# Optimization experiments

Measured on AMD Instinct MI355X. Metric: run time of the kernel, lower is better.

## Reference

```python
import jax, jax.numpy as jnp
import numpy as np

NUM_PTS = 4
N_OFF = 4


def inverse_sigmoid(x, eps=1e-5):
    x = jnp.clip(x, 0.0, 1.0)
    return jnp.log(jnp.clip(x, eps, None) / jnp.clip(1.0 - x, eps, None))


def uniform_flat_indices(T, H, W, n):
    # torch: linspace(hop/2, D-1-hop/2, n).round().long(), meshed over (t,h,w)
    def ax(D):
        hop = D / n
        return jnp.round(jnp.linspace(hop / 2.0, D - 1.0 - hop / 2.0, n)).astype(jnp.int32)
    ti, hi, wi = ax(T), ax(H), ax(W)
    return ((ti[:, None, None] * H + hi[None, :, None]) * W + wi[None, None, :]).reshape(-1)


def _normalized_thw(idx, T, H, W):
    wn = (idx % W).astype(jnp.float32) / (W - 1)
    hn = ((idx // W) % H).astype(jnp.float32) / (H - 1)
    tn = (idx // (W * H)).astype(jnp.float32) / (T - 1)
    return jnp.stack([tn, hn, wn], axis=-1)


def grid_sample_3d(inp, grid):
    # Matches torch F.grid_sample 5D, bilinear, padding zeros, align_corners=False.
    # inp: (N,C,D,H,W); grid: (N,Do,Ho,Wo,3) with grid[...,0]=x->W, 1=y->H, 2=z->D
    N, C, D, H, W = inp.shape
    Do, Ho, Wo = grid.shape[1:4]
    P = Do * Ho * Wo
    g = grid.reshape(N, P, 3)
    ix = ((g[..., 0] + 1.0) * W - 1.0) * 0.5
    iy = ((g[..., 1] + 1.0) * H - 1.0) * 0.5
    iz = ((g[..., 2] + 1.0) * D - 1.0) * 0.5
    x0 = jnp.floor(ix); y0 = jnp.floor(iy); z0 = jnp.floor(iz)
    fx = ix - x0; fy = iy - y0; fz = iz - z0
    x0i = x0.astype(jnp.int32); y0i = y0.astype(jnp.int32); z0i = z0.astype(jnp.int32)
    inp_flat = inp.reshape(N, C, D * H * W)
    out = jnp.zeros((N, C, P), inp.dtype)
    for dz in (0, 1):
        for dy in (0, 1):
            for dx in (0, 1):
                xi = x0i + dx; yi = y0i + dy; zi = z0i + dz
                w = (fx if dx else 1.0 - fx) * (fy if dy else 1.0 - fy) * (fz if dz else 1.0 - fz)
                valid = (xi >= 0) & (xi < W) & (yi >= 0) & (yi < H) & (zi >= 0) & (zi < D)
                flat = (jnp.clip(zi, 0, D - 1) * H + jnp.clip(yi, 0, H - 1)) * W + jnp.clip(xi, 0, W - 1)
                vals = jnp.take_along_axis(inp_flat, jnp.broadcast_to(flat[:, None, :], (N, C, P)), axis=2)
                out = out + vals * (w * valid.astype(inp.dtype))[:, None, :]
    return out.reshape(N, C, Do, Ho, Wo)


def forward(features, pos, W1, b1, W2, b2, Wn, bn, Wl, bl, Woff, boff, Ww, bw, gamma, beta):
    B, C, T, H, Wd, L = features.shape
    THW = T * H * Wd
    No = N_OFF
    N = NUM_PTS ** 3
    d = C // No
    BLNo = B * L * No

    flat = uniform_flat_indices(T, H, Wd, NUM_PTS)                    # (N,)
    ind_pts = jnp.broadcast_to(flat[None, None, :], (B, L, N))

    feats_l = jnp.transpose(features, (0, 5, 2, 3, 4, 1)).reshape(B, L, THW, C)
    pos_l = jnp.transpose(pos, (0, 5, 2, 3, 4, 1)).reshape(B, L, THW, C)
    sampled_pts = feats_l[:, :, flat, :]                              # (B,L,N,C)
    sampled_pos = pos_l[:, :, flat, :]
    glob = jnp.transpose(jnp.mean(features, axis=(2, 3, 4)), (0, 2, 1))  # (B,L,C)
    glob = jnp.broadcast_to(glob[:, :, None, :], (B, L, N, C))

    off_src = jnp.concatenate([sampled_pts, sampled_pos, glob], axis=-1)
    off_src = jax.nn.relu(off_src @ W1 + b1)
    off_src = jax.nn.relu(off_src @ W2 + b2)                          # (B,L,N,C)

    nxt = off_src @ Wn + bn                                           # (B,L,N,3)
    w_l = jax.nn.softmax(off_src @ Wl + bl, axis=-1)                  # (B,L,N,L)

    osr = off_src.reshape(B, L, N, No, d).transpose(0, 1, 3, 2, 4).reshape(BLNo, N, d)
    offset = osr @ Woff + boff                                        # (BLNo,N,3)
    w_o = jax.nn.softmax(osr @ Ww + bw, axis=-1)[..., 1:]             # (BLNo,N,1)

    # --- build flow field: identity grid with sampled coords scattered in ---
    idx = jnp.broadcast_to(ind_pts[:, :, None, :], (B, L, No, N)).reshape(BLNo, N)
    thw = _normalized_thw(idx, T, H, Wd)
    samp = jax.nn.sigmoid(inverse_sigmoid(thw) + offset) * 2.0 - 1.0  # (BLNo,N,3)
    mesh = jnp.stack(jnp.meshgrid(jnp.linspace(-1.0, 1.0, T), jnp.linspace(-1.0, 1.0, H), jnp.linspace(-1.0, 1.0, Wd), indexing='ij'), axis=-1).reshape(THW, 3)
    base = jnp.broadcast_to(mesh[None], (BLNo, THW, 3))
    bI = jnp.arange(BLNo)[:, None]
    flow = base.at[bI, idx].set(samp).reshape(BLNo, T, H, Wd, 3)

    feats_rep = jnp.transpose(features, (0, 5, 1, 2, 3, 4))           # (B,L,C,T,H,W)
    feats_rep = jnp.broadcast_to(feats_rep[:, :, None], (B, L, No, C, T, H, Wd)).reshape(BLNo, C, T, H, Wd)
    sf = grid_sample_3d(feats_rep, flow)                              # (BLNo,C,T,H,W)
    sf = jnp.transpose(sf, (0, 2, 3, 4, 1))                           # (BLNo,T,H,W,C)

    wo_full = jnp.zeros((BLNo, THW, 1), features.dtype).at[bI, idx].set(w_o).reshape(BLNo, T, H, Wd, 1)
    wsf = (sf * wo_full).reshape(B, L, No, T, H, Wd, C).sum(axis=2)   # (B,L,T,H,W,C)
    feats2 = features + jnp.transpose(wsf, (0, 5, 2, 3, 4, 1))        # (B,C,T,H,W,L)

    # level weights scattered then summed over target-level axis l
    bI2 = jnp.arange(B)[:, None, None]
    lI2 = jnp.arange(L)[None, :, None]
    wl_full = jnp.zeros((B, L, THW, L), features.dtype).at[bI2, lI2, ind_pts].set(w_l)
    wl_sum = wl_full.sum(axis=-1).reshape(B, L, T, H, Wd)             # (B,L,T,H,W)
    feats3 = feats2 * jnp.transpose(wl_sum, (0, 2, 3, 4, 1))[:, None] # broadcast over C

    # LayerNorm over channel dim (transpose(1,-1) in torch)
    x = jnp.transpose(feats3, (0, 5, 2, 3, 4, 1))                     # (B,L,T,H,W,C)
    mu = jnp.mean(x, axis=-1, keepdims=True)
    var = jnp.var(x, axis=-1, keepdims=True)
    xn = (x - mu) * jax.lax.rsqrt(var + 1e-5) * gamma + beta
    feats_out = jnp.transpose(xn, (0, 5, 2, 3, 4, 1))

    # offset_adder -> next flattened indices
    thw2 = _normalized_thw(ind_pts, T, H, Wd)
    disp = jax.nn.sigmoid(inverse_sigmoid(thw2) + nxt)
    scale = jnp.array([T - 1, H - 1, Wd - 1], jnp.float32)
    di = jnp.round(disp * scale).astype(jnp.int32)
    next_ind = H * Wd * di[..., 0] + Wd * di[..., 1] + di[..., 2]
    return feats_out, next_ind


def setup_inputs():
    key = jax.random.key(0)
    ks = jax.random.split(key, 10)
    B, C, T, H, W, L = 1, 256, 8, 32, 32, 4
    s = 0.02
    d = C // N_OFF
    return {
        'features': jax.random.normal(ks[0], (B, C, T, H, W, L), jnp.float32),
        'pos': jax.random.normal(ks[1], (B, C, T, H, W, L), jnp.float32),
        'W1': jax.random.normal(ks[2], (3 * C, C), jnp.float32) * s,
        'b1': jnp.zeros((C,), jnp.float32),
        'W2': jax.random.normal(ks[3], (C, C), jnp.float32) * s,
        'b2': jnp.zeros((C,), jnp.float32),
        'Wn': jax.random.normal(ks[4], (C, 3), jnp.float32) * s,
        'bn': jnp.zeros((3,), jnp.float32),
        'Wl': jax.random.normal(ks[5], (C, L), jnp.float32) * s,
        'bl': jnp.zeros((L,), jnp.float32),
        'Woff': jax.random.normal(ks[6], (d, 3), jnp.float32) * s,
        'boff': jnp.zeros((3,), jnp.float32),
        'Ww': jax.random.normal(ks[7], (d, 2), jnp.float32) * s,
        'bw': jnp.zeros((2,), jnp.float32),
        'gamma': jnp.ones((C,), jnp.float32),
        'beta': jnp.zeros((C,), jnp.float32),
    }


def reference(features, pos, W1, b1, W2, b2, Wn, bn, Wl, bl, Woff, boff, Ww, bw, gamma, beta):
    return forward(features, pos, W1, b1, W2, b2, Wn, bn, Wl, bl, Woff, boff, Ww, bw, gamma, beta)
```

## Files before the change

kernel.cpp:

```cpp
#include <hip/hip_runtime.h>
#include <math.h>

#define CDIM 256
#define TDIM 8
#define HDIM 32
#define WDIM 32
#define LDIM 4
#define THW 8192
#define CSTR 32768
#define NS 64
#define OUT0_SIZE 8388608

__device__ __constant__ int c_ti[4] = {1, 3, 4, 6};
__device__ __constant__ int c_hw[4] = {4, 12, 19, 27};

__device__ __forceinline__ float sigm(float x) { return 1.f / (1.f + expf(-x)); }

__device__ __forceinline__ float wave_sum64(float x) {
#pragma unroll
    for (int s = 32; s > 0; s >>= 1) x += __shfl_xor(x, s, 64);
    return x;
}

__global__ void __launch_bounds__(256)
k_fill_part(const float* __restrict__ feat, const float* __restrict__ beta,
            float* __restrict__ out, float4* __restrict__ partF) {
    int c = blockIdx.x >> 3, part = blockIdx.x & 7;
    float bv = beta[c];
    float4 bf = make_float4(bv, bv, bv, bv);
    const float4* f = (const float4*)(feat + (size_t)c * CSTR) + part * 1024;
    float4* o = (float4*)(out + (size_t)c * CSTR) + part * 1024;
    float4 a = make_float4(0.f, 0.f, 0.f, 0.f);
#pragma unroll
    for (int it = 0; it < 4; ++it) {
        int i = it * 256 + threadIdx.x;
        float4 v = f[i];
        o[i] = bf;
        a.x += v.x; a.y += v.y; a.z += v.z; a.w += v.w;
    }
#pragma unroll
    for (int s = 32; s > 0; s >>= 1) {
        a.x += __shfl_xor(a.x, s, 64);
        a.y += __shfl_xor(a.y, s, 64);
        a.z += __shfl_xor(a.z, s, 64);
        a.w += __shfl_xor(a.w, s, 64);
    }
    __shared__ float4 sw[4];
    if ((threadIdx.x & 63) == 0) sw[threadIdx.x >> 6] = a;
    __syncthreads();
    if (threadIdx.x == 0) {
        float4 r;
        r.x = sw[0].x + sw[1].x + sw[2].x + sw[3].x;
        r.y = sw[0].y + sw[1].y + sw[2].y + sw[3].y;
        r.z = sw[0].z + sw[1].z + sw[2].z + sw[3].z;
        r.w = sw[0].w + sw[1].w + sw[2].w + sw[3].w;
        partF[blockIdx.x] = r;
    }
}

__global__ void __launch_bounds__(256)
k_gather(const float* __restrict__ feat, const float* __restrict__ pos,
         const float4* __restrict__ partF, float* __restrict__ in1T) {
    int m = blockIdx.x, l = m >> 6, n = m & 63;
    int sp = (c_ti[n >> 4] * HDIM + c_hw[(n >> 2) & 3]) * WDIM + c_hw[n & 3];
    int t = threadIdx.x;
    in1T[(size_t)t * 256 + m] = feat[(size_t)t * CSTR + sp * LDIM + l];
    in1T[(size_t)(256 + t) * 256 + m] = pos[(size_t)t * CSTR + sp * LDIM + l];
    float s = 0.f;
#pragma unroll
    for (int p = 0; p < 8; ++p) {
        float4 v = partF[t * 8 + p];
        s += (l == 0) ? v.x : (l == 1) ? v.y : (l == 2) ? v.z : v.w;
    }
    in1T[(size_t)(512 + t) * 256 + m] = s * (1.f / 8192.f);
}

template <int KITER, int WRITE_T>
__global__ void __launch_bounds__(256)
k_gemm(const float* __restrict__ AT, const float* __restrict__ Wt,
       const float* __restrict__ bias, float* __restrict__ outp) {
    __shared__ float sAcc[256][33];
    int mt = blockIdx.x >> 4, jt = blockIdx.x & 15;
    int m0 = mt * 16, j0 = jt * 16;
    int t = threadIdx.x;
    int j8 = t & 7, kq = t >> 3;
    int j = j0 + j8 * 2;
    float acc0[16], acc1[16];
#pragma unroll
    for (int i = 0; i < 16; ++i) { acc0[i] = 0.f; acc1[i] = 0.f; }
#pragma unroll 4
    for (int kk = 0; kk < KITER; ++kk) {
        int k = kq + (kk << 5);
        const float4* ap = (const float4*)(AT + (size_t)k * 256 + m0);
        float av[16];
        ((float4*)av)[0] = ap[0];
        ((float4*)av)[1] = ap[1];
        ((float4*)av)[2] = ap[2];
        ((float4*)av)[3] = ap[3];
        float2 w = *(const float2*)(Wt + (size_t)k * 256 + j);
#pragma unroll
        for (int i = 0; i < 16; ++i) {
            acc0[i] = fmaf(av[i], w.x, acc0[i]);
            acc1[i] = fmaf(av[i], w.y, acc1[i]);
        }
    }
#pragma unroll
    for (int i = 0; i < 16; ++i) {
        sAcc[i * 16 + j8 * 2 + 0][kq] = acc0[i];
        sAcc[i * 16 + j8 * 2 + 1][kq] = acc1[i];
    }
    __syncthreads();
    int i = t >> 4, jj = t & 15;
    float v = bias[j0 + jj];
#pragma unroll
    for (int q = 0; q < 32; ++q) v += sAcc[t][q];
    v = fmaxf(v, 0.f);
    if (WRITE_T)
        outp[(size_t)(j0 + jj) * 256 + m0 + i] = v;
    else
        outp[(size_t)(m0 + i) * 256 + j0 + jj] = v;
}

__global__ void __launch_bounds__(256)
k_heads_sample(const float* __restrict__ feat, const float* __restrict__ osrc,
               const float* __restrict__ Wn, const float* __restrict__ bn,
               const float* __restrict__ Woff, const float* __restrict__ boff,
               const float* __restrict__ Ww, const float* __restrict__ bw,
               const float* __restrict__ gamma, const float* __restrict__ beta,
               float* __restrict__ out, float* __restrict__ next_out) {
    __shared__ float s_samp[4][3];
    __shared__ float s_wo[4];
    __shared__ float s_w[32];
    __shared__ int   s_o[32];
    __shared__ float red1[4], red2[4], redn[3][4];

    int m = blockIdx.x, l = m >> 6, n = m & 63;
    int j = threadIdx.x, o = j >> 6, r = j & 63;

    float v = osrc[(size_t)m * 256 + j];

    float pn0 = wave_sum64(v * Wn[j * 3 + 0]);
    float pn1 = wave_sum64(v * Wn[j * 3 + 1]);
    float pn2 = wave_sum64(v * Wn[j * 3 + 2]);
    if (r == 0) { redn[0][o] = pn0; redn[1][o] = pn1; redn[2][o] = pn2; }

    float po0 = wave_sum64(v * Woff[r * 3 + 0]);
    float po1 = wave_sum64(v * Woff[r * 3 + 1]);
    float po2 = wave_sum64(v * Woff[r * 3 + 2]);
    float z0  = wave_sum64(v * Ww[r * 2 + 0]);
    float z1  = wave_sum64(v * Ww[r * 2 + 1]);

    float tn = (float)c_ti[n >> 4] / 7.f;
    float hn = (float)c_hw[(n >> 2) & 3] / 31.f;
    float wn = (float)c_hw[n & 3] / 31.f;
    float lg0 = logf(tn / (1.f - tn));
    float lg1 = logf(hn / (1.f - hn));
    float lg2 = logf(wn / (1.f - wn));

    if (r == 0) {
        s_samp[o][0] = sigm(lg0 + po0 + boff[0]) * 2.f - 1.f;
        s_samp[o][1] = sigm(lg1 + po1 + boff[1]) * 2.f - 1.f;
        s_samp[o][2] = sigm(lg2 + po2 + boff[2]) * 2.f - 1.f;
        s_wo[o] = 1.f / (1.f + expf((z0 + bw[0]) - (z1 + bw[1])));
    }
    __syncthreads();

    if (j == 0) {
        float t0 = redn[0][0] + redn[0][1] + redn[0][2] + redn[0][3];
        float t1 = redn[1][0] + redn[1][1] + redn[1][2] + redn[1][3];
        float t2 = redn[2][0] + redn[2][1] + redn[2][2] + redn[2][3];
        float d0 = rintf(sigm(lg0 + t0 + bn[0]) * 7.f);
        float d1 = rintf(sigm(lg1 + t1 + bn[1]) * 31.f);
        float d2 = rintf(sigm(lg2 + t2 + bn[2]) * 31.f);
        next_out[m] = 1024.f * d0 + 32.f * d1 + d2;
    }

    if (j < 4) {
        int oo = j;
        float wv = s_wo[oo];
        float g0 = s_samp[oo][0], g1 = s_samp[oo][1], g2 = s_samp[oo][2];
        float ix = ((g0 + 1.f) * 32.f - 1.f) * 0.5f;
        float iy = ((g1 + 1.f) * 32.f - 1.f) * 0.5f;
        float iz = ((g2 + 1.f) * 8.f  - 1.f) * 0.5f;
        float x0f = floorf(ix), y0f = floorf(iy), z0f = floorf(iz);
        float fx = ix - x0f, fy = iy - y0f, fz = iz - z0f;
        int x0 = (int)x0f, y0 = (int)y0f, z0 = (int)z0f;
#pragma unroll
        for (int k = 0; k < 8; ++k) {
            int dx = k & 1, dy = (k >> 1) & 1, dz = k >> 2;
            int xi = x0 + dx, yi = y0 + dy, zi = z0 + dz;
            float w = (dx ? fx : 1.f - fx) * (dy ? fy : 1.f - fy) * (dz ? fz : 1.f - fz);
            bool valid = (xi >= 0) && (xi < WDIM) && (yi >= 0) && (yi < HDIM) && (zi >= 0) && (zi < TDIM);
            int xc = min(max(xi, 0), WDIM - 1);
            int yc = min(max(yi, 0), HDIM - 1);
            int zc = min(max(zi, 0), TDIM - 1);
            s_w[oo * 8 + k] = valid ? w * wv : 0.f;
            s_o[oo * 8 + k] = ((zc * HDIM + yc) * WDIM + xc) * LDIM + l;
        }
    }
    __syncthreads();

    int c = j;
    const float* fc = feat + (size_t)c * CSTR;
    int sp = (c_ti[n >> 4] * HDIM + c_hw[(n >> 2) & 3]) * WDIM + c_hw[n & 3];
    float acc = fc[sp * LDIM + l];
#pragma unroll
    for (int k = 0; k < 32; ++k) acc += s_w[k] * fc[s_o[k]];

    float s1 = acc, s2 = acc * acc;
#pragma unroll
    for (int d = 32; d > 0; d >>= 1) { s1 += __shfl_xor(s1, d, 64); s2 += __shfl_xor(s2, d, 64); }
    int wid = j >> 6;
    if ((j & 63) == 0) { red1[wid] = s1; red2[wid] = s2; }
    __syncthreads();
    float tot  = red1[0] + red1[1] + red1[2] + red1[3];
    float totq = red2[0] + red2[1] + red2[2] + red2[3];
    float mu = tot * (1.f / 256.f);
    float var = fmaxf(totq * (1.f / 256.f) - mu * mu, 0.f);
    float y = (acc - mu) * rsqrtf(var + 1e-5f) * gamma[c] + beta[c];
    out[(size_t)c * CSTR + sp * LDIM + l] = y;
}

extern "C" void kernel_launch(void* const* d_in, const int* in_sizes, int n_in,
                              void* d_out, int out_size, void* d_ws, size_t ws_size,
                              hipStream_t stream) {
    const float* feat = (const float*)d_in[0];
    const float* pos  = (const float*)d_in[1];
    const float* W1   = (const float*)d_in[2];
    const float* b1   = (const float*)d_in[3];
    const float* W2   = (const float*)d_in[4];
    const float* b2   = (const float*)d_in[5];
    const float* Wn   = (const float*)d_in[6];
    const float* bn   = (const float*)d_in[7];
    const float* Woff = (const float*)d_in[10];
    const float* boff = (const float*)d_in[11];
    const float* Ww   = (const float*)d_in[12];
    const float* bw   = (const float*)d_in[13];
    const float* gamma= (const float*)d_in[14];
    const float* beta = (const float*)d_in[15];
    float* out = (float*)d_out;
    float* next_out = out + OUT0_SIZE;

    float* ws    = (float*)d_ws;
    float4* partF= (float4*)ws;
    float* in1T  = ws + 8192;
    float* h1T   = in1T + 196608;
    float* osrc  = h1T + 65536;

    k_fill_part<<<2048, 256, 0, stream>>>(feat, beta, out, partF);
    k_gather<<<256, 256, 0, stream>>>(feat, pos, partF, in1T);
    k_gemm<24, 1><<<256, 256, 0, stream>>>(in1T, W1, b1, h1T);
    k_gemm<8, 0><<<256, 256, 0, stream>>>(h1T, W2, b2, osrc);
    k_heads_sample<<<256, 256, 0, stream>>>(feat, osrc, Wn, bn, Woff, boff, Ww, bw,
                                            gamma, beta, out, next_out);
}
```

Before: 159.5 us.

## Fuse gather, two GEMMs and heads into one cooperative kernel with grid syncs

Four small 256-block launches (gather, two GEMM phases, heads/sampling) are merged into a single cooperative kernel that uses grid-wide barriers between phases. The goal is to remove the per-launch overhead and inter-kernel gaps between these short stages. In exchange, each grid sync carries its own cost, and the fused kernel uses the union of the shared-memory footprints, which could limit occupancy. The cooperative launch requires all 256 blocks to be resident at once, which 256 CUs make feasible.

```diff
diff --git a/kernel.cpp b/kernel.cpp
--- a/kernel.cpp
+++ b/kernel.cpp
@@ -1,5 +1,8 @@
 #include <hip/hip_runtime.h>
+#include <hip/hip_cooperative_groups.h>
 #include <math.h>
+
+namespace cg = cooperative_groups;
 
 #define CDIM 256
 #define TDIM 8
@@ -58,28 +61,12 @@
     }
 }
 
-__global__ void __launch_bounds__(256)
-k_gather(const float* __restrict__ feat, const float* __restrict__ pos,
-         const float4* __restrict__ partF, float* __restrict__ in1T) {
-    int m = blockIdx.x, l = m >> 6, n = m & 63;
-    int sp = (c_ti[n >> 4] * HDIM + c_hw[(n >> 2) & 3]) * WDIM + c_hw[n & 3];
-    int t = threadIdx.x;
-    in1T[(size_t)t * 256 + m] = feat[(size_t)t * CSTR + sp * LDIM + l];
-    in1T[(size_t)(256 + t) * 256 + m] = pos[(size_t)t * CSTR + sp * LDIM + l];
-    float s = 0.f;
-#pragma unroll
-    for (int p = 0; p < 8; ++p) {
-        float4 v = partF[t * 8 + p];
-        s += (l == 0) ? v.x : (l == 1) ? v.y : (l == 2) ? v.z : v.w;
-    }
-    in1T[(size_t)(512 + t) * 256 + m] = s * (1.f / 8192.f);
-}
-
 template <int KITER, int WRITE_T>
-__global__ void __launch_bounds__(256)
-k_gemm(const float* __restrict__ AT, const float* __restrict__ Wt,
-       const float* __restrict__ bias, float* __restrict__ outp) {
-    __shared__ float sAcc[256][33];
+__device__ __forceinline__ void gemm_phase(const float* __restrict__ AT,
+                                           const float* __restrict__ Wt,
+                                           const float* __restrict__ bias,
+                                           float* __restrict__ outp,
+                                           float sAcc[256][33]) {
     int mt = blockIdx.x >> 4, jt = blockIdx.x & 15;
     int m0 = mt * 16, j0 = jt * 16;
     int t = threadIdx.x;
@@ -122,103 +109,133 @@
 }
 
 __global__ void __launch_bounds__(256)
-k_heads_sample(const float* __restrict__ feat, const float* __restrict__ osrc,
-               const float* __restrict__ Wn, const float* __restrict__ bn,
-               const float* __restrict__ Woff, const float* __restrict__ boff,
-               const float* __restrict__ Ww, const float* __restrict__ bw,
-               const float* __restrict__ gamma, const float* __restrict__ beta,
-               float* __restrict__ out, float* __restrict__ next_out) {
+k_fused(const float* __restrict__ feat, const float* __restrict__ pos,
+        const float4* __restrict__ partF,
+        const float* __restrict__ W1, const float* __restrict__ b1,
+        const float* __restrict__ W2, const float* __restrict__ b2,
+        const float* __restrict__ Wn, const float* __restrict__ bn,
+        const float* __restrict__ Woff, const float* __restrict__ boff,
+        const float* __restrict__ Ww, const float* __restrict__ bw,
+        const float* __restrict__ gamma, const float* __restrict__ beta,
+        float* __restrict__ in1T, float* __restrict__ h1T, float* __restrict__ osrc,
+        float* __restrict__ out, float* __restrict__ next_out) {
+    cg::grid_group grid = cg::this_grid();
+
+    __shared__ float sAcc[256][33];
     __shared__ float s_samp[4][3];
     __shared__ float s_wo[4];
     __shared__ float s_w[32];
     __shared__ int   s_o[32];
     __shared__ float red1[4], red2[4], redn[3][4];
 
-    int m = blockIdx.x, l = m >> 6, n = m & 63;
-    int j = threadIdx.x, o = j >> 6, r = j & 63;
-
-    float v = osrc[(size_t)m * 256 + j];
-
-    float pn0 = wave_sum64(v * Wn[j * 3 + 0]);
-    float pn1 = wave_sum64(v * Wn[j * 3 + 1]);
-    float pn2 = wave_sum64(v * Wn[j * 3 + 2]);
-    if (r == 0) { redn[0][o] = pn0; redn[1][o] = pn1; redn[2][o] = pn2; }
-
-    float po0 = wave_sum64(v * Woff[r * 3 + 0]);
-    float po1 = wave_sum64(v * Woff[r * 3 + 1]);
-    float po2 = wave_sum64(v * Woff[r * 3 + 2]);
-    float z0  = wave_sum64(v * Ww[r * 2 + 0]);
-    float z1  = wave_sum64(v * Ww[r * 2 + 1]);
-
-    float tn = (float)c_ti[n >> 4] / 7.f;
-    float hn = (float)c_hw[(n >> 2) & 3] / 31.f;
-    float wn = (float)c_hw[n & 3] / 31.f;
-    float lg0 = logf(tn / (1.f - tn));
-    float lg1 = logf(hn / (1.f - hn));
-    float lg2 = logf(wn / (1.f - wn));
-
-    if (r == 0) {
-        s_samp[o][0] = sigm(lg0 + po0 + boff[0]) * 2.f - 1.f;
-        s_samp[o][1] = sigm(lg1 + po1 + boff[1]) * 2.f - 1.f;
-        s_samp[o][2] = sigm(lg2 + po2 + boff[2]) * 2.f - 1.f;
-        s_wo[o] = 1.f / (1.f + expf((z0 + bw[0]) - (z1 + bw[1])));
-    }
-    __syncthreads();
-
-    if (j == 0) {
-        float t0 = redn[0][0] + redn[0][1] + redn[0][2] + redn[0][3];
-        float t1 = redn[1][0] + redn[1][1] + redn[1][2] + redn[1][3];
-        float t2 = redn[2][0] + redn[2][1] + redn[2][2] + redn[2][3];
-        float d0 = rintf(sigm(lg0 + t0 + bn[0]) * 7.f);
-        float d1 = rintf(sigm(lg1 + t1 + bn[1]) * 31.f);
-        float d2 = rintf(sigm(lg2 + t2 + bn[2]) * 31.f);
-        next_out[m] = 1024.f * d0 + 32.f * d1 + d2;
-    }
-
-    if (j < 4) {
-        int oo = j;
-        float wv = s_wo[oo];
-        float g0 = s_samp[oo][0], g1 = s_samp[oo][1], g2 = s_samp[oo][2];
-        float ix = ((g0 + 1.f) * 32.f - 1.f) * 0.5f;
-        float iy = ((g1 + 1.f) * 32.f - 1.f) * 0.5f;
-        float iz = ((g2 + 1.f) * 8.f  - 1.f) * 0.5f;
-        float x0f = floorf(ix), y0f = floorf(iy), z0f = floorf(iz);
-        float fx = ix - x0f, fy = iy - y0f, fz = iz - z0f;
-        int x0 = (int)x0f, y0 = (int)y0f, z0 = (int)z0f;
-#pragma unroll
-        for (int k = 0; k < 8; ++k) {
-            int dx = k & 1, dy = (k >> 1) & 1, dz = k >> 2;
-            int xi = x0 + dx, yi = y0 + dy, zi = z0 + dz;
-            float w = (dx ? fx : 1.f - fx) * (dy ? fy : 1.f - fy) * (dz ? fz : 1.f - fz);
-            bool valid = (xi >= 0) && (xi < WDIM) && (yi >= 0) && (yi < HDIM) && (zi >= 0) && (zi < TDIM);
-            int xc = min(max(xi, 0), WDIM - 1);
-            int yc = min(max(yi, 0), HDIM - 1);
-            int zc = min(max(zi, 0), TDIM - 1);
-            s_w[oo * 8 + k] = valid ? w * wv : 0.f;
-            s_o[oo * 8 + k] = ((zc * HDIM + yc) * WDIM + xc) * LDIM + l;
-        }
-    }
-    __syncthreads();
-
-    int c = j;
-    const float* fc = feat + (size_t)c * CSTR;
-    int sp = (c_ti[n >> 4] * HDIM + c_hw[(n >> 2) & 3]) * WDIM + c_hw[n & 3];
-    float acc = fc[sp * LDIM + l];
-#pragma unroll
-    for (int k = 0; k < 32; ++k) acc += s_w[k] * fc[s_o[k]];
-
-    float s1 = acc, s2 = acc * acc;
-#pragma unroll
-    for (int d = 32; d > 0; d >>= 1) { s1 += __shfl_xor(s1, d, 64); s2 += __shfl_xor(s2, d, 64); }
-    int wid = j >> 6;
-    if ((j & 63) == 0) { red1[wid] = s1; red2[wid] = s2; }
-    __syncthreads();
-    float tot  = red1[0] + red1[1] + red1[2] + red1[3];
-    float totq = red2[0] + red2[1] + red2[2] + red2[3];
-    float mu = tot * (1.f / 256.f);
-    float var = fmaxf(totq * (1.f / 256.f) - mu * mu, 0.f);
-    float y = (acc - mu) * rsqrtf(var + 1e-5f) * gamma[c] + beta[c];
-    out[(size_t)c * CSTR + sp * LDIM + l] = y;
+    const int m = blockIdx.x, l = m >> 6, n = m & 63;
+    const int sp = (c_ti[n >> 4] * HDIM + c_hw[(n >> 2) & 3]) * WDIM + c_hw[n & 3];
+
+    {
+        int t = threadIdx.x;
+        in1T[(size_t)t * 256 + m] = feat[(size_t)t * CSTR + sp * LDIM + l];
+        in1T[(size_t)(256 + t) * 256 + m] = pos[(size_t)t * CSTR + sp * LDIM + l];
+        float s = 0.f;
+#pragma unroll
+        for (int p = 0; p < 8; ++p) {
+            float4 v = partF[t * 8 + p];
+            s += (l == 0) ? v.x : (l == 1) ? v.y : (l == 2) ? v.z : v.w;
+        }
+        in1T[(size_t)(512 + t) * 256 + m] = s * (1.f / 8192.f);
+    }
+    grid.sync();
+
+    gemm_phase<24, 1>(in1T, W1, b1, h1T, sAcc);
+    grid.sync();
+
+    gemm_phase<8, 0>(h1T, W2, b2, osrc, sAcc);
+    grid.sync();
+
+    {
+        int j = threadIdx.x, o = j >> 6, r = j & 63;
+
+        float v = osrc[(size_t)m * 256 + j];
+
+        float pn0 = wave_sum64(v * Wn[j * 3 + 0]);
+        float pn1 = wave_sum64(v * Wn[j * 3 + 1]);
+        float pn2 = wave_sum64(v * Wn[j * 3 + 2]);
+        if (r == 0) { redn[0][o] = pn0; redn[1][o] = pn1; redn[2][o] = pn2; }
+
+        float po0 = wave_sum64(v * Woff[r * 3 + 0]);
+        float po1 = wave_sum64(v * Woff[r * 3 + 1]);
+        float po2 = wave_sum64(v * Woff[r * 3 + 2]);
+        float z0  = wave_sum64(v * Ww[r * 2 + 0]);
+        float z1  = wave_sum64(v * Ww[r * 2 + 1]);
+
+        float tn = (float)c_ti[n >> 4] / 7.f;
+        float hn = (float)c_hw[(n >> 2) & 3] / 31.f;
+        float wn = (float)c_hw[n & 3] / 31.f;
+        float lg0 = logf(tn / (1.f - tn));
+        float lg1 = logf(hn / (1.f - hn));
+        float lg2 = logf(wn / (1.f - wn));
+
+        if (r == 0) {
+            s_samp[o][0] = sigm(lg0 + po0 + boff[0]) * 2.f - 1.f;
+            s_samp[o][1] = sigm(lg1 + po1 + boff[1]) * 2.f - 1.f;
+            s_samp[o][2] = sigm(lg2 + po2 + boff[2]) * 2.f - 1.f;
+            s_wo[o] = 1.f / (1.f + expf((z0 + bw[0]) - (z1 + bw[1])));
+        }
+        __syncthreads();
+
+        if (j == 0) {
+            float t0 = redn[0][0] + redn[0][1] + redn[0][2] + redn[0][3];
+            float t1 = redn[1][0] + redn[1][1] + redn[1][2] + redn[1][3];
+            float t2 = redn[2][0] + redn[2][1] + redn[2][2] + redn[2][3];
+            float d0 = rintf(sigm(lg0 + t0 + bn[0]) * 7.f);
+            float d1 = rintf(sigm(lg1 + t1 + bn[1]) * 31.f);
+            float d2 = rintf(sigm(lg2 + t2 + bn[2]) * 31.f);
+            next_out[m] = 1024.f * d0 + 32.f * d1 + d2;
+        }
+
+        if (j < 4) {
+            int oo = j;
+            float wv = s_wo[oo];
+            float g0 = s_samp[oo][0], g1 = s_samp[oo][1], g2 = s_samp[oo][2];
+            float ix = ((g0 + 1.f) * 32.f - 1.f) * 0.5f;
+            float iy = ((g1 + 1.f) * 32.f - 1.f) * 0.5f;
+            float iz = ((g2 + 1.f) * 8.f  - 1.f) * 0.5f;
+            float x0f = floorf(ix), y0f = floorf(iy), z0f = floorf(iz);
+            float fx = ix - x0f, fy = iy - y0f, fz = iz - z0f;
+            int x0 = (int)x0f, y0 = (int)y0f, z0 = (int)z0f;
+#pragma unroll
+            for (int k = 0; k < 8; ++k) {
+                int dx = k & 1, dy = (k >> 1) & 1, dz = k >> 2;
+                int xi = x0 + dx, yi = y0 + dy, zi = z0 + dz;
+                float w = (dx ? fx : 1.f - fx) * (dy ? fy : 1.f - fy) * (dz ? fz : 1.f - fz);
+                bool valid = (xi >= 0) && (xi < WDIM) && (yi >= 0) && (yi < HDIM) && (zi >= 0) && (zi < TDIM);
+                int xc = min(max(xi, 0), WDIM - 1);
+                int yc = min(max(yi, 0), HDIM - 1);
+                int zc = min(max(zi, 0), TDIM - 1);
+                s_w[oo * 8 + k] = valid ? w * wv : 0.f;
+                s_o[oo * 8 + k] = ((zc * HDIM + yc) * WDIM + xc) * LDIM + l;
+            }
+        }
+        __syncthreads();
+
+        int c = j;
+        const float* fc = feat + (size_t)c * CSTR;
+        float acc = fc[sp * LDIM + l];
+#pragma unroll
+        for (int k = 0; k < 32; ++k) acc += s_w[k] * fc[s_o[k]];
+
+        float s1 = acc, s2 = acc * acc;
+#pragma unroll
+        for (int d = 32; d > 0; d >>= 1) { s1 += __shfl_xor(s1, d, 64); s2 += __shfl_xor(s2, d, 64); }
+        int wid = j >> 6;
+        if ((j & 63) == 0) { red1[wid] = s1; red2[wid] = s2; }
+        __syncthreads();
+        float tot  = red1[0] + red1[1] + red1[2] + red1[3];
+        float totq = red2[0] + red2[1] + red2[2] + red2[3];
+        float mu = tot * (1.f / 256.f);
+        float var = fmaxf(totq * (1.f / 256.f) - mu * mu, 0.f);
+        float y = (acc - mu) * rsqrtf(var + 1e-5f) * gamma[c] + beta[c];
+        out[(size_t)c * CSTR + sp * LDIM + l] = y;
+    }
 }
 
 extern "C" void kernel_launch(void* const* d_in, const int* in_sizes, int n_in,
@@ -248,9 +265,10 @@
     float* osrc  = h1T + 65536;
 
     k_fill_part<<<2048, 256, 0, stream>>>(feat, beta, out, partF);
-    k_gather<<<256, 256, 0, stream>>>(feat, pos, partF, in1T);
-    k_gemm<24, 1><<<256, 256, 0, stream>>>(in1T, W1, b1, h1T);
-    k_gemm<8, 0><<<256, 256, 0, stream>>>(h1T, W2, b2, osrc);
-    k_heads_sample<<<256, 256, 0, stream>>>(feat, osrc, Wn, bn, Woff, boff, Ww, bw,
-                                            gamma, beta, out, next_out);
-}
+
+    void* args[] = {&feat, &pos, &partF, &W1, &b1, &W2, &b2, &Wn, &bn,
+                    &Woff, &boff, &Ww, &bw, &gamma, &beta,
+                    &in1T, &h1T, &osrc, &out, &next_out};
+    hipLaunchCooperativeKernel(reinterpret_cast<void*>(k_fused),
+                               dim3(256), dim3(256), args, 0, stream);
+}
```

Result: slower. 278.5 us (+74.6%).

## Coalesce gather writes, stage GEMM A tiles in LDS, split sampling across 512 threads

Applied to the files above, without the earlier changes.

The gather kernel now maps blocks to rows of the transposed input and threads to samples, so each store to in1T is coalesced, and it launches 768 blocks instead of 256. The GEMM copies each 256x16 chunk of A into padded shared memory with coalesced float4 loads before the FMA loop, replacing repeated global reads. The heads/sample kernel uses 512 threads and splits the 32 trilinear gathers per channel across two halves, issuing all loads first to raise memory-level parallelism. The cost is extra barriers and shared memory, and the whole pipeline is likely dominated by the k_fill_part pass over the full tensor, which is unchanged.

```diff
diff --git a/kernel.cpp b/kernel.cpp
--- a/kernel.cpp
+++ b/kernel.cpp
@@ -61,24 +61,33 @@
 __global__ void __launch_bounds__(256)
 k_gather(const float* __restrict__ feat, const float* __restrict__ pos,
          const float4* __restrict__ partF, float* __restrict__ in1T) {
-    int m = blockIdx.x, l = m >> 6, n = m & 63;
+    int k = blockIdx.x;
+    int m = threadIdx.x;
+    int l = m >> 6, n = m & 63;
     int sp = (c_ti[n >> 4] * HDIM + c_hw[(n >> 2) & 3]) * WDIM + c_hw[n & 3];
-    int t = threadIdx.x;
-    in1T[(size_t)t * 256 + m] = feat[(size_t)t * CSTR + sp * LDIM + l];
-    in1T[(size_t)(256 + t) * 256 + m] = pos[(size_t)t * CSTR + sp * LDIM + l];
-    float s = 0.f;
-#pragma unroll
-    for (int p = 0; p < 8; ++p) {
-        float4 v = partF[t * 8 + p];
-        s += (l == 0) ? v.x : (l == 1) ? v.y : (l == 2) ? v.z : v.w;
-    }
-    in1T[(size_t)(512 + t) * 256 + m] = s * (1.f / 8192.f);
+    float val;
+    if (k < 256) {
+        val = feat[(size_t)k * CSTR + sp * LDIM + l];
+    } else if (k < 512) {
+        val = pos[(size_t)(k - 256) * CSTR + sp * LDIM + l];
+    } else {
+        int c = k - 512;
+        float s = 0.f;
+#pragma unroll
+        for (int p = 0; p < 8; ++p) {
+            float4 v = partF[c * 8 + p];
+            s += (l == 0) ? v.x : (l == 1) ? v.y : (l == 2) ? v.z : v.w;
+        }
+        val = s * (1.f / 8192.f);
+    }
+    in1T[(size_t)k * 256 + m] = val;
 }
 
 template <int KITER, int WRITE_T>
 __global__ void __launch_bounds__(256)
 k_gemm(const float* __restrict__ AT, const float* __restrict__ Wt,
        const float* __restrict__ bias, float* __restrict__ outp) {
+    __shared__ float aLds[256 * 20];
     __shared__ float sAcc[256][33];
     int mt = blockIdx.x >> 4, jt = blockIdx.x & 15;
     int m0 = mt * 16, j0 = jt * 16;
@@ -88,22 +97,37 @@
     float acc0[16], acc1[16];
 #pragma unroll
     for (int i = 0; i < 16; ++i) { acc0[i] = 0.f; acc1[i] = 0.f; }
-#pragma unroll 4
-    for (int kk = 0; kk < KITER; ++kk) {
-        int k = kq + (kk << 5);
-        const float4* ap = (const float4*)(AT + (size_t)k * 256 + m0);
-        float av[16];
-        ((float4*)av)[0] = ap[0];
-        ((float4*)av)[1] = ap[1];
-        ((float4*)av)[2] = ap[2];
-        ((float4*)av)[3] = ap[3];
-        float2 w = *(const float2*)(Wt + (size_t)k * 256 + j);
-#pragma unroll
-        for (int i = 0; i < 16; ++i) {
-            acc0[i] = fmaf(av[i], w.x, acc0[i]);
-            acc1[i] = fmaf(av[i], w.y, acc1[i]);
-        }
-    }
+
+    constexpr int NCHUNK = KITER / 8;
+    for (int ch = 0; ch < NCHUNK; ++ch) {
+        if (ch) __syncthreads();
+#pragma unroll
+        for (int i = 0; i < 4; ++i) {
+            int idx = i * 256 + t;
+            int k = idx >> 2, mq = idx & 3;
+            *(float4*)(&aLds[k * 20 + mq * 4]) =
+                *(const float4*)(AT + (size_t)(ch * 256 + k) * 256 + m0 + mq * 4);
+        }
+        __syncthreads();
+#pragma unroll
+        for (int kk2 = 0; kk2 < 8; ++kk2) {
+            int kl = kq + (kk2 << 5);
+            int kg = ch * 256 + kl;
+            const float* ar = &aLds[kl * 20];
+            float av[16];
+            ((float4*)av)[0] = *(const float4*)(ar + 0);
+            ((float4*)av)[1] = *(const float4*)(ar + 4);
+            ((float4*)av)[2] = *(const float4*)(ar + 8);
+            ((float4*)av)[3] = *(const float4*)(ar + 12);
+            float2 w = *(const float2*)(Wt + (size_t)kg * 256 + j);
+#pragma unroll
+            for (int i = 0; i < 16; ++i) {
+                acc0[i] = fmaf(av[i], w.x, acc0[i]);
+                acc1[i] = fmaf(av[i], w.y, acc1[i]);
+            }
+        }
+    }
+    __syncthreads();
 #pragma unroll
     for (int i = 0; i < 16; ++i) {
         sAcc[i * 16 + j8 * 2 + 0][kq] = acc0[i];
@@ -121,7 +145,7 @@
         outp[(size_t)(m0 + i) * 256 + j0 + jj] = v;
 }
 
-__global__ void __launch_bounds__(256)
+__global__ void __launch_bounds__(512)
 k_heads_sample(const float* __restrict__ feat, const float* __restrict__ osrc,
                const float* __restrict__ Wn, const float* __restrict__ bn,
                const float* __restrict__ Woff, const float* __restrict__ boff,
@@ -133,39 +157,49 @@
     __shared__ float s_w[32];
     __shared__ int   s_o[32];
     __shared__ float red1[4], red2[4], redn[3][4];
+    __shared__ float sPa[2][256];
 
     int m = blockIdx.x, l = m >> 6, n = m & 63;
-    int j = threadIdx.x, o = j >> 6, r = j & 63;
-
-    float v = osrc[(size_t)m * 256 + j];
-
-    float pn0 = wave_sum64(v * Wn[j * 3 + 0]);
-    float pn1 = wave_sum64(v * Wn[j * 3 + 1]);
-    float pn2 = wave_sum64(v * Wn[j * 3 + 2]);
-    if (r == 0) { redn[0][o] = pn0; redn[1][o] = pn1; redn[2][o] = pn2; }
-
-    float po0 = wave_sum64(v * Woff[r * 3 + 0]);
-    float po1 = wave_sum64(v * Woff[r * 3 + 1]);
-    float po2 = wave_sum64(v * Woff[r * 3 + 2]);
-    float z0  = wave_sum64(v * Ww[r * 2 + 0]);
-    float z1  = wave_sum64(v * Ww[r * 2 + 1]);
-
-    float tn = (float)c_ti[n >> 4] / 7.f;
-    float hn = (float)c_hw[(n >> 2) & 3] / 31.f;
-    float wn = (float)c_hw[n & 3] / 31.f;
-    float lg0 = logf(tn / (1.f - tn));
-    float lg1 = logf(hn / (1.f - hn));
-    float lg2 = logf(wn / (1.f - wn));
-
-    if (r == 0) {
-        s_samp[o][0] = sigm(lg0 + po0 + boff[0]) * 2.f - 1.f;
-        s_samp[o][1] = sigm(lg1 + po1 + boff[1]) * 2.f - 1.f;
-        s_samp[o][2] = sigm(lg2 + po2 + boff[2]) * 2.f - 1.f;
-        s_wo[o] = 1.f / (1.f + expf((z0 + bw[0]) - (z1 + bw[1])));
-    }
-    __syncthreads();
-
-    if (j == 0) {
+    int t = threadIdx.x;
+    int sp = (c_ti[n >> 4] * HDIM + c_hw[(n >> 2) & 3]) * WDIM + c_hw[n & 3];
+
+    if (t < 256) {
+        int j = t, o = j >> 6, r = j & 63;
+        float v = osrc[(size_t)m * 256 + j];
+
+        float pn0 = wave_sum64(v * Wn[j * 3 + 0]);
+        float pn1 = wave_sum64(v * Wn[j * 3 + 1]);
+        float pn2 = wave_sum64(v * Wn[j * 3 + 2]);
+        if (r == 0) { redn[0][o] = pn0; redn[1][o] = pn1; redn[2][o] = pn2; }
+
+        float po0 = wave_sum64(v * Woff[r * 3 + 0]);
+        float po1 = wave_sum64(v * Woff[r * 3 + 1]);
+        float po2 = wave_sum64(v * Woff[r * 3 + 2]);
+        float z0  = wave_sum64(v * Ww[r * 2 + 0]);
+        float z1  = wave_sum64(v * Ww[r * 2 + 1]);
+
+        if (r == 0) {
+            float tn = (float)c_ti[n >> 4] / 7.f;
+            float hn = (float)c_hw[(n >> 2) & 3] / 31.f;
+            float wn = (float)c_hw[n & 3] / 31.f;
+            float lg0 = logf(tn / (1.f - tn));
+            float lg1 = logf(hn / (1.f - hn));
+            float lg2 = logf(wn / (1.f - wn));
+            s_samp[o][0] = sigm(lg0 + po0 + boff[0]) * 2.f - 1.f;
+            s_samp[o][1] = sigm(lg1 + po1 + boff[1]) * 2.f - 1.f;
+            s_samp[o][2] = sigm(lg2 + po2 + boff[2]) * 2.f - 1.f;
+            s_wo[o] = 1.f / (1.f + expf((z0 + bw[0]) - (z1 + bw[1])));
+        }
+    }
+    __syncthreads();
+
+    if (t == 0) {
+        float tn = (float)c_ti[n >> 4] / 7.f;
+        float hn = (float)c_hw[(n >> 2) & 3] / 31.f;
+        float wn = (float)c_hw[n & 3] / 31.f;
+        float lg0 = logf(tn / (1.f - tn));
+        float lg1 = logf(hn / (1.f - hn));
+        float lg2 = logf(wn / (1.f - wn));
         float t0 = redn[0][0] + redn[0][1] + redn[0][2] + redn[0][3];
         float t1 = redn[1][0] + redn[1][1] + redn[1][2] + redn[1][3];
         float t2 = redn[2][0] + redn[2][1] + redn[2][2] + redn[2][3];
@@ -175,8 +209,8 @@
         next_out[m] = 1024.f * d0 + 32.f * d1 + d2;
     }
 
-    if (j < 4) {
-        int oo = j;
+    if (t < 4) {
+        int oo = t;
         float wv = s_wo[oo];
         float g0 = s_samp[oo][0], g1 = s_samp[oo][1], g2 = s_samp[oo][2];
         float ix = ((g0 + 1.f) * 32.f - 1.f) * 0.5f;
@@ -200,25 +234,39 @@
     }
     __syncthreads();
 
-    int c = j;
-    const float* fc = feat + (size_t)c * CSTR;
-    int sp = (c_ti[n >> 4] * HDIM + c_hw[(n >> 2) & 3]) * WDIM + c_hw[n & 3];
-    float acc = fc[sp * LDIM + l];
-#pragma unroll
-    for (int k = 0; k < 32; ++k) acc += s_w[k] * fc[s_o[k]];
-
-    float s1 = acc, s2 = acc * acc;
-#pragma unroll
-    for (int d = 32; d > 0; d >>= 1) { s1 += __shfl_xor(s1, d, 64); s2 += __shfl_xor(s2, d, 64); }
-    int wid = j >> 6;
-    if ((j & 63) == 0) { red1[wid] = s1; red2[wid] = s2; }
-    __syncthreads();
-    float tot  = red1[0] + red1[1] + red1[2] + red1[3];
-    float totq = red2[0] + red2[1] + red2[2] + red2[3];
-    float mu = tot * (1.f / 256.f);
-    float var = fmaxf(totq * (1.f / 256.f) - mu * mu, 0.f);
-    float y = (acc - mu) * rsqrtf(var + 1e-5f) * gamma[c] + beta[c];
-    out[(size_t)c * CSTR + sp * LDIM + l] = y;
+    {
+        int c = t & 255, h = t >> 8;
+        const float* fc = feat + (size_t)c * CSTR;
+        float vals[16];
+        int base = h * 16;
+#pragma unroll
+        for (int k = 0; k < 16; ++k) vals[k] = fc[s_o[base + k]];
+        float acc = (h == 0) ? fc[sp * LDIM + l] : 0.f;
+#pragma unroll
+        for (int k = 0; k < 16; ++k) acc += s_w[base + k] * vals[k];
+        sPa[h][c] = acc;
+    }
+    __syncthreads();
+
+    float accf = 0.f;
+    if (t < 256) {
+        accf = sPa[0][t] + sPa[1][t];
+        float s1 = accf, s2 = accf * accf;
+#pragma unroll
+        for (int d = 32; d > 0; d >>= 1) { s1 += __shfl_xor(s1, d, 64); s2 += __shfl_xor(s2, d, 64); }
+        int wid = t >> 6;
+        if ((t & 63) == 0) { red1[wid] = s1; red2[wid] = s2; }
+    }
+    __syncthreads();
+    if (t < 256) {
+        int c = t;
+        float tot  = red1[0] + red1[1] + red1[2] + red1[3];
+        float totq = red2[0] + red2[1] + red2[2] + red2[3];
+        float mu = tot * (1.f / 256.f);
+        float var = fmaxf(totq * (1.f / 256.f) - mu * mu, 0.f);
+        float y = (accf - mu) * rsqrtf(var + 1e-5f) * gamma[c] + beta[c];
+        out[(size_t)c * CSTR + sp * LDIM + l] = y;
+    }
 }
 
 extern "C" void kernel_launch(void* const* d_in, const int* in_sizes, int n_in,
@@ -248,9 +296,9 @@
     float* osrc  = h1T + 65536;
 
     k_fill_part<<<2048, 256, 0, stream>>>(feat, beta, out, partF);
-    k_gather<<<256, 256, 0, stream>>>(feat, pos, partF, in1T);
+    k_gather<<<768, 256, 0, stream>>>(feat, pos, partF, in1T);
     k_gemm<24, 1><<<256, 256, 0, stream>>>(in1T, W1, b1, h1T);
     k_gemm<8, 0><<<256, 256, 0, stream>>>(h1T, W2, b2, osrc);
-    k_heads_sample<<<256, 256, 0, stream>>>(feat, osrc, Wn, bn, Woff, boff, Ww, bw,
+    k_heads_sample<<<256, 512, 0, stream>>>(feat, osrc, Wn, bn, Woff, boff, Ww, bw,
                                             gamma, beta, out, next_out);
 }
```

After: 153.7 us. -3.6%, faster.
